# Optimization experiments

Hardware: AMD Instinct MI355X
Metric: run time of the kernel (lower is better)

The kernel has to match this reference:

```python
import jax, jax.numpy as jnp
import numpy as np


def _dense_image_warp(image, flow):
    """Faithful JAX port of tfa.image.dense_image_warp.

    image: [B,H,W,C] float, flow: [B,H,W,2] float (flow[...,0]=dy, flow[...,1]=dx).
    query point (y,x) = grid(y,x) - flow; bilinear interp with TFA's clamping:
    floor clipped to [0, size-2], alpha clipped to [0,1].
    """
    B, H, W, C = image.shape
    gy, gx = jnp.meshgrid(
        jnp.arange(H, dtype=flow.dtype), jnp.arange(W, dtype=flow.dtype), indexing="ij"
    )
    qy = gy[None] - flow[..., 0]  # [B,H,W]
    qx = gx[None] - flow[..., 1]

    y0f = jnp.clip(jnp.floor(qy), 0.0, H - 2)
    x0f = jnp.clip(jnp.floor(qx), 0.0, W - 2)
    ay = jnp.clip(qy - y0f, 0.0, 1.0)[..., None]  # [B,H,W,1]
    ax = jnp.clip(qx - x0f, 0.0, 1.0)[..., None]

    y0 = y0f.astype(jnp.int32)
    x0 = x0f.astype(jnp.int32)
    b = jnp.arange(B, dtype=jnp.int32)[:, None, None]

    tl = image[b, y0, x0]          # top-left  [B,H,W,C]
    tr = image[b, y0, x0 + 1]      # top-right
    bl = image[b, y0 + 1, x0]      # bottom-left
    br = image[b, y0 + 1, x0 + 1]  # bottom-right

    top = tl + ax * (tr - tl)
    bot = bl + ax * (br - bl)
    return top + ay * (bot - top)


def setup_inputs() -> dict:
    key = jax.random.key(0)
    k1, k2 = jax.random.split(key)
    B, H, W, C = 8, 1024, 768, 3
    image = jax.random.normal(k1, (B, H, W, C), dtype=jnp.float32)
    # flow magnitudes of a few pixels, typical for appearance-flow warping
    flow = jax.random.normal(k2, (B, H, W, 2), dtype=jnp.float32) * 5.0
    return {"image": image, "flow": flow}


def reference(image, flow):
    return _dense_image_warp(image, flow)
```

## Files before the change

kernel.cpp:

```cpp
#include <hip/hip_runtime.h>


constexpr int B = 8;
constexpr int H = 1024;
constexpr int W = 768;
constexpr int C = 3;

constexpr int TY = 32, TX = 32;
constexpr int WIN_ROWS = 65;
constexpr int WIN_COLS = 64;
constexpr int WSTRIDE = WIN_COLS * C;
constexpr int CHUNKS  = WIN_ROWS * (WSTRIDE / 4);
constexpr int TILES_X = W / TX;
constexpr int TILES_Y = H / TY;
constexpr int TILES_PER_B = TILES_X * TILES_Y;

constexpr int NTHREADS = 512;
constexpr int PX_PER_T = (TY * TX) / NTHREADS;

typedef float vfloat2 __attribute__((ext_vector_type(2)));
typedef float vfloat4 __attribute__((ext_vector_type(4)));
typedef float vfloat2_a4 __attribute__((ext_vector_type(2), aligned(4)));
typedef float vfloat4_a4 __attribute__((ext_vector_type(4), aligned(4)));

__global__ __launch_bounds__(NTHREADS, 6) void warp_kernel(
    const float* __restrict__ image,
    const float* __restrict__ flow,
    float* __restrict__ out)
{
    __shared__ float win[WIN_ROWS * WSTRIDE + 64];

    const int flat = blockIdx.x;
    const int b    = flat & 7;
    const int s    = flat >> 3;
    const int ty   = s / TILES_X;
    const int tx   = s - ty * TILES_X;
    const int Y0 = ty * TY, X0 = tx * TX;

    const int rowLo = min(max(Y0 - 16, 0), H - WIN_ROWS);
    const int colLo = min(max((X0 - 15) & ~3, 0), W - WIN_COLS);

    const int lane = threadIdx.x & 63;
    const int wv   = threadIdx.x >> 6;

    const float* gwin = image + ((size_t)b * H + rowLo) * (W * C) + colLo * C;
#pragma unroll 1
    for (int j = wv; j * 64 < CHUNKS; j += 8) {
        int ci = j * 64 + lane;
        if (ci >= CHUNKS) ci = CHUNKS - 1;
        const int r = ci / 48;
        const int c = ci - r * 48;
        const float* g = gwin + (size_t)r * (W * C) + c * 4;
        __builtin_amdgcn_global_load_lds(
            (const __attribute__((address_space(1))) void*)g,
            (__attribute__((address_space(3))) void*)(win + (size_t)j * 256),
            16, 0, 0);
    }

    vfloat2 f[PX_PER_T];
#pragma unroll
    for (int k = 0; k < PX_PER_T; ++k) {
        const int p   = threadIdx.x + k * NTHREADS;
        const int py  = p >> 5;
        const int pxx = p & 31;
        const size_t pix = ((size_t)b * H + (Y0 + py)) * W + (X0 + pxx);
        f[k] = __builtin_nontemporal_load((const vfloat2*)flow + pix);
    }

    __syncthreads();

#pragma unroll
    for (int k = 0; k < PX_PER_T; ++k) {
        const int p   = threadIdx.x + k * NTHREADS;
        const int py  = p >> 5;
        const int pxx = p & 31;
        const int y = Y0 + py;
        const int x = X0 + pxx;
        const size_t pix = ((size_t)b * H + y) * W + x;

        const float qy = (float)y - f[k].x;
        const float qx = (float)x - f[k].y;

        float y0f = floorf(qy);
        float x0f = floorf(qx);
        y0f = fminf(fmaxf(y0f, 0.0f), (float)(H - 2));
        x0f = fminf(fmaxf(x0f, 0.0f), (float)(W - 2));
        const float ay = fminf(fmaxf(qy - y0f, 0.0f), 1.0f);
        const float ax = fminf(fmaxf(qx - x0f, 0.0f), 1.0f);

        const int y0 = (int)y0f;
        const int x0 = (int)x0f;

        float tl0, tl1, tl2, tr0, tr1, tr2, bl0, bl1, bl2, br0, br1, br2;

        const bool inwin = (y0 >= rowLo) & (y0 <= rowLo + WIN_ROWS - 2) &
                           (x0 >= colLo) & (x0 <= colLo + WIN_COLS - 2);
        if (inwin) {
            const float* t = &win[(y0 - rowLo) * WSTRIDE + (x0 - colLo) * C];
            tl0 = t[0]; tl1 = t[1]; tl2 = t[2];
            tr0 = t[3]; tr1 = t[4]; tr2 = t[5];
            const float* bo = t + WSTRIDE;
            bl0 = bo[0]; bl1 = bo[1]; bl2 = bo[2];
            br0 = bo[3]; br1 = bo[4]; br2 = bo[5];
        } else {
            const float* top = image + (((size_t)b * H + y0) * W + x0) * C;
            const float* bot = top + (size_t)W * C;
            const vfloat4 t4 = *(const vfloat4_a4*)top;
            const vfloat2 t2 = *(const vfloat2_a4*)(top + 4);
            const vfloat4 b4 = *(const vfloat4_a4*)bot;
            const vfloat2 b2 = *(const vfloat2_a4*)(bot + 4);
            tl0 = t4.x; tl1 = t4.y; tl2 = t4.z;
            tr0 = t4.w; tr1 = t2.x; tr2 = t2.y;
            bl0 = b4.x; bl1 = b4.y; bl2 = b4.z;
            br0 = b4.w; br1 = b2.x; br2 = b2.y;
        }

        const float tp0 = tl0 + ax * (tr0 - tl0);
        const float tp1 = tl1 + ax * (tr1 - tl1);
        const float tp2 = tl2 + ax * (tr2 - tl2);
        const float bo0 = bl0 + ax * (br0 - bl0);
        const float bo1 = bl1 + ax * (br1 - bl1);
        const float bo2 = bl2 + ax * (br2 - bl2);

        float* o = out + pix * C;
        __builtin_nontemporal_store(tp0 + ay * (bo0 - tp0), &o[0]);
        __builtin_nontemporal_store(tp1 + ay * (bo1 - tp1), &o[1]);
        __builtin_nontemporal_store(tp2 + ay * (bo2 - tp2), &o[2]);
    }
}

extern "C" void kernel_launch(void* const* d_in, const int* in_sizes, int n_in,
                              void* d_out, int out_size, void* d_ws, size_t ws_size,
                              hipStream_t stream) {
    const float* image = (const float*)d_in[0];
    const float* flow  = (const float*)d_in[1];
    float* out = (float*)d_out;

    dim3 grid(B * TILES_PER_B);
    dim3 block(NTHREADS);
    warp_kernel<<<grid, block, 0, stream>>>(image, flow, out);
}
```

Measured before the change: 176.1 us.

## Stream column strips through an LDS ring buffer with prefetched row bands

```diff
diff --git a/kernel.cpp b/kernel.cpp
--- a/kernel.cpp
+++ b/kernel.cpp
@@ -6,80 +6,91 @@
 constexpr int W = 768;
 constexpr int C = 3;
 
-constexpr int TY = 32, TX = 32;
-constexpr int WIN_ROWS = 65;
+constexpr int TY = 32;
+constexpr int TX = 24;
+constexpr int TILES_Y = H / TY;
+constexpr int COLS_X  = W / TX;
+
 constexpr int WIN_COLS = 64;
-constexpr int WSTRIDE = WIN_COLS * C;
-constexpr int CHUNKS  = WIN_ROWS * (WSTRIDE / 4);
-constexpr int TILES_X = W / TX;
-constexpr int TILES_Y = H / TY;
-constexpr int TILES_PER_B = TILES_X * TILES_Y;
+constexpr int WSF = WIN_COLS * C;
+constexpr int ROW_CHUNKS = WSF / 4;
+constexpr int BAND = TY;
+constexpr int RING_ROWS = 4 * BAND;
+constexpr int BAND_GROUPS = BAND * ROW_CHUNKS / 64;
+constexpr int NTHREADS = TY * TX;
+constexpr int NWAVES = NTHREADS / 64;
+constexpr int GPW = BAND_GROUPS / NWAVES;
 
-constexpr int NTHREADS = 512;
-constexpr int PX_PER_T = (TY * TX) / NTHREADS;
+static_assert(GPW * NWAVES == BAND_GROUPS, "uniform staging required for vmcnt");
 
 typedef float vfloat2 __attribute__((ext_vector_type(2)));
 typedef float vfloat4 __attribute__((ext_vector_type(4)));
 typedef float vfloat2_a4 __attribute__((ext_vector_type(2), aligned(4)));
 typedef float vfloat4_a4 __attribute__((ext_vector_type(4), aligned(4)));
 
-__global__ __launch_bounds__(NTHREADS, 6) void warp_kernel(
+__global__ __launch_bounds__(NTHREADS) void warp_kernel(
     const float* __restrict__ image,
     const float* __restrict__ flow,
     float* __restrict__ out)
 {
-    __shared__ float win[WIN_ROWS * WSTRIDE + 64];
+    __shared__ float win[RING_ROWS * WSF];
 
-    const int flat = blockIdx.x;
-    const int b    = flat & 7;
-    const int s    = flat >> 3;
-    const int ty   = s / TILES_X;
-    const int tx   = s - ty * TILES_X;
-    const int Y0 = ty * TY, X0 = tx * TX;
-
-    const int rowLo = min(max(Y0 - 16, 0), H - WIN_ROWS);
-    const int colLo = min(max((X0 - 15) & ~3, 0), W - WIN_COLS);
+    const int b  = blockIdx.x & 7;
+    const int tx = blockIdx.x >> 3;
+    const int X0 = tx * TX;
+    const int colLo = min(max(X0 - 20, 0), W - WIN_COLS);
 
     const int lane = threadIdx.x & 63;
     const int wv   = threadIdx.x >> 6;
 
-    const float* gwin = image + ((size_t)b * H + rowLo) * (W * C) + colLo * C;
+    const int py  = threadIdx.x / TX;
+    const int pxx = threadIdx.x - py * TX;
+    const int xg  = X0 + pxx;
+    const float xgf = (float)xg;
+
+    const float* gcol = image + (size_t)b * H * (W * C) + colLo * C;
+
+    auto stage_band = [&](int k) {
+        const int slotBase = (k & 3) * BAND;
+#pragma unroll
+        for (int i = 0; i < GPW; ++i) {
+            const int j  = i * NWAVES + wv;
+            const int ci = j * 64 + lane;
+            const int r  = ci / ROW_CHUNKS;
+            const int c  = ci - r * ROW_CHUNKS;
+            const int rimg = min(k * BAND + r, H - 1);
+            const float* g = gcol + (size_t)rimg * (W * C) + c * 4;
+            __builtin_amdgcn_global_load_lds(
+                (const __attribute__((address_space(1))) void*)g,
+                (__attribute__((address_space(3))) void*)(win + slotBase * WSF + j * 256),
+                16, 0, 0);
+        }
+    };
+
+    auto load_flow = [&](int t) -> vfloat2 {
+        const int yf = min(t * TY + py, H - 1);
+        return __builtin_nontemporal_load(
+            (const vfloat2*)flow + (((size_t)b * H + yf) * W + xg));
+    };
+
+    stage_band(0);
+    stage_band(1);
+    vfloat2 fcur = load_flow(0);
+
 #pragma unroll 1
-    for (int j = wv; j * 64 < CHUNKS; j += 8) {
-        int ci = j * 64 + lane;
-        if (ci >= CHUNKS) ci = CHUNKS - 1;
-        const int r = ci / 48;
-        const int c = ci - r * 48;
-        const float* g = gwin + (size_t)r * (W * C) + c * 4;
-        __builtin_amdgcn_global_load_lds(
-            (const __attribute__((address_space(1))) void*)g,
-            (__attribute__((address_space(3))) void*)(win + (size_t)j * 256),
-            16, 0, 0);
-    }
+    for (int t = 0; t < TILES_Y; ++t) {
+        stage_band(t + 2);
+        const vfloat2 fnxt = load_flow(t + 1);
 
-    vfloat2 f[PX_PER_T];
-#pragma unroll
-    for (int k = 0; k < PX_PER_T; ++k) {
-        const int p   = threadIdx.x + k * NTHREADS;
-        const int py  = p >> 5;
-        const int pxx = p & 31;
-        const size_t pix = ((size_t)b * H + (Y0 + py)) * W + (X0 + pxx);
-        f[k] = __builtin_nontemporal_load((const vfloat2*)flow + pix);
-    }
+        asm volatile("s_waitcnt vmcnt(3)" ::: "memory");
+        __builtin_amdgcn_s_barrier();
+        __builtin_amdgcn_sched_barrier(0);
 
-    __syncthreads();
+        const int Y0 = t * TY;
+        const int y  = Y0 + py;
 
-#pragma unroll
-    for (int k = 0; k < PX_PER_T; ++k) {
-        const int p   = threadIdx.x + k * NTHREADS;
-        const int py  = p >> 5;
-        const int pxx = p & 31;
-        const int y = Y0 + py;
-        const int x = X0 + pxx;
-        const size_t pix = ((size_t)b * H + y) * W + x;
-
-        const float qy = (float)y - f[k].x;
-        const float qx = (float)x - f[k].y;
+        const float qy = (float)y - fcur.x;
+        const float qx = xgf      - fcur.y;
 
         float y0f = floorf(qy);
         float x0f = floorf(qx);
@@ -87,21 +98,20 @@
         x0f = fminf(fmaxf(x0f, 0.0f), (float)(W - 2));
         const float ay = fminf(fmaxf(qy - y0f, 0.0f), 1.0f);
         const float ax = fminf(fmaxf(qx - x0f, 0.0f), 1.0f);
-
         const int y0 = (int)y0f;
         const int x0 = (int)x0f;
 
         float tl0, tl1, tl2, tr0, tr1, tr2, bl0, bl1, bl2, br0, br1, br2;
 
-        const bool inwin = (y0 >= rowLo) & (y0 <= rowLo + WIN_ROWS - 2) &
+        const bool inwin = (y0 >= Y0 - BAND) & (y0 <= Y0 + 2 * BAND - 2) &
                            (x0 >= colLo) & (x0 <= colLo + WIN_COLS - 2);
         if (inwin) {
-            const float* t = &win[(y0 - rowLo) * WSTRIDE + (x0 - colLo) * C];
-            tl0 = t[0]; tl1 = t[1]; tl2 = t[2];
-            tr0 = t[3]; tr1 = t[4]; tr2 = t[5];
-            const float* bo = t + WSTRIDE;
-            bl0 = bo[0]; bl1 = bo[1]; bl2 = bo[2];
-            br0 = bo[3]; br1 = bo[4]; br2 = bo[5];
+            const float* tp = &win[(y0 & (RING_ROWS - 1)) * WSF + (x0 - colLo) * C];
+            const float* bp = &win[((y0 + 1) & (RING_ROWS - 1)) * WSF + (x0 - colLo) * C];
+            tl0 = tp[0]; tl1 = tp[1]; tl2 = tp[2];
+            tr0 = tp[3]; tr1 = tp[4]; tr2 = tp[5];
+            bl0 = bp[0]; bl1 = bp[1]; bl2 = bp[2];
+            br0 = bp[3]; br1 = bp[4]; br2 = bp[5];
         } else {
             const float* top = image + (((size_t)b * H + y0) * W + x0) * C;
             const float* bot = top + (size_t)W * C;
@@ -122,10 +132,14 @@
         const float bo1 = bl1 + ax * (br1 - bl1);
         const float bo2 = bl2 + ax * (br2 - bl2);
 
-        float* o = out + pix * C;
+        float* o = out + (((size_t)b * H + y) * W + xg) * C;
         __builtin_nontemporal_store(tp0 + ay * (bo0 - tp0), &o[0]);
         __builtin_nontemporal_store(tp1 + ay * (bo1 - tp1), &o[1]);
         __builtin_nontemporal_store(tp2 + ay * (bo2 - tp2), &o[2]);
+
+        __builtin_amdgcn_s_barrier();
+        __builtin_amdgcn_sched_barrier(0);
+        fcur = fnxt;
     }
 }
 
@@ -136,7 +150,7 @@
     const float* flow  = (const float*)d_in[1];
     float* out = (float*)d_out;
 
-    dim3 grid(B * TILES_PER_B);
+    dim3 grid(B * COLS_X);
     dim3 block(NTHREADS);
     warp_kernel<<<grid, block, 0, stream>>>(image, flow, out);
 }
```

New measurement: 192.1 us. 1.09x slower.

## Drop LDS window staging and gather bilinear corners directly from global memory

Applied to the files above, without the earlier changes.

```diff
diff --git a/kernel.cpp b/kernel.cpp
--- a/kernel.cpp
+++ b/kernel.cpp
@@ -7,10 +7,6 @@
 constexpr int C = 3;
 
 constexpr int TY = 32, TX = 32;
-constexpr int WIN_ROWS = 65;
-constexpr int WIN_COLS = 64;
-constexpr int WSTRIDE = WIN_COLS * C;
-constexpr int CHUNKS  = WIN_ROWS * (WSTRIDE / 4);
 constexpr int TILES_X = W / TX;
 constexpr int TILES_Y = H / TY;
 constexpr int TILES_PER_B = TILES_X * TILES_Y;
@@ -23,13 +19,11 @@
 typedef float vfloat2_a4 __attribute__((ext_vector_type(2), aligned(4)));
 typedef float vfloat4_a4 __attribute__((ext_vector_type(4), aligned(4)));
 
-__global__ __launch_bounds__(NTHREADS, 6) void warp_kernel(
+__global__ __launch_bounds__(NTHREADS, 8) void warp_kernel(
     const float* __restrict__ image,
     const float* __restrict__ flow,
     float* __restrict__ out)
 {
-    __shared__ float win[WIN_ROWS * WSTRIDE + 64];
-
     const int flat = blockIdx.x;
     const int b    = flat & 7;
     const int s    = flat >> 3;
@@ -37,95 +31,59 @@
     const int tx   = s - ty * TILES_X;
     const int Y0 = ty * TY, X0 = tx * TX;
 
-    const int rowLo = min(max(Y0 - 16, 0), H - WIN_ROWS);
-    const int colLo = min(max((X0 - 15) & ~3, 0), W - WIN_COLS);
+    const float* imgB = image + (size_t)b * H * (W * C);
 
-    const int lane = threadIdx.x & 63;
-    const int wv   = threadIdx.x >> 6;
-
-    const float* gwin = image + ((size_t)b * H + rowLo) * (W * C) + colLo * C;
-#pragma unroll 1
-    for (int j = wv; j * 64 < CHUNKS; j += 8) {
-        int ci = j * 64 + lane;
-        if (ci >= CHUNKS) ci = CHUNKS - 1;
-        const int r = ci / 48;
-        const int c = ci - r * 48;
-        const float* g = gwin + (size_t)r * (W * C) + c * 4;
-        __builtin_amdgcn_global_load_lds(
-            (const __attribute__((address_space(1))) void*)g,
-            (__attribute__((address_space(3))) void*)(win + (size_t)j * 256),
-            16, 0, 0);
-    }
-
+    int yy[PX_PER_T], xx[PX_PER_T];
     vfloat2 f[PX_PER_T];
 #pragma unroll
     for (int k = 0; k < PX_PER_T; ++k) {
-        const int p   = threadIdx.x + k * NTHREADS;
-        const int py  = p >> 5;
-        const int pxx = p & 31;
-        const size_t pix = ((size_t)b * H + (Y0 + py)) * W + (X0 + pxx);
-        f[k] = __builtin_nontemporal_load((const vfloat2*)flow + pix);
+        const int p = threadIdx.x + k * NTHREADS;
+        yy[k] = Y0 + (p >> 5);
+        xx[k] = X0 + (p & 31);
+        f[k] = __builtin_nontemporal_load(
+            (const vfloat2*)flow + (((size_t)b * H + yy[k]) * W + xx[k]));
     }
 
-    __syncthreads();
-
+    vfloat4 t4[PX_PER_T], b4[PX_PER_T];
+    vfloat2 t2[PX_PER_T], b2[PX_PER_T];
+    float ax[PX_PER_T], ay[PX_PER_T];
 #pragma unroll
     for (int k = 0; k < PX_PER_T; ++k) {
-        const int p   = threadIdx.x + k * NTHREADS;
-        const int py  = p >> 5;
-        const int pxx = p & 31;
-        const int y = Y0 + py;
-        const int x = X0 + pxx;
-        const size_t pix = ((size_t)b * H + y) * W + x;
-
-        const float qy = (float)y - f[k].x;
-        const float qx = (float)x - f[k].y;
-
+        const float qy = (float)yy[k] - f[k].x;
+        const float qx = (float)xx[k] - f[k].y;
         float y0f = floorf(qy);
         float x0f = floorf(qx);
         y0f = fminf(fmaxf(y0f, 0.0f), (float)(H - 2));
         x0f = fminf(fmaxf(x0f, 0.0f), (float)(W - 2));
-        const float ay = fminf(fmaxf(qy - y0f, 0.0f), 1.0f);
-        const float ax = fminf(fmaxf(qx - x0f, 0.0f), 1.0f);
+        ay[k] = fminf(fmaxf(qy - y0f, 0.0f), 1.0f);
+        ax[k] = fminf(fmaxf(qx - x0f, 0.0f), 1.0f);
 
-        const int y0 = (int)y0f;
-        const int x0 = (int)x0f;
+        const float* top = imgB + ((size_t)(int)y0f * W + (int)x0f) * C;
+        const float* bot = top + (size_t)W * C;
+        t4[k] = *(const vfloat4_a4*)top;
+        t2[k] = *(const vfloat2_a4*)(top + 4);
+        b4[k] = *(const vfloat4_a4*)bot;
+        b2[k] = *(const vfloat2_a4*)(bot + 4);
+    }
 
-        float tl0, tl1, tl2, tr0, tr1, tr2, bl0, bl1, bl2, br0, br1, br2;
+#pragma unroll
+    for (int k = 0; k < PX_PER_T; ++k) {
+        const float tl0 = t4[k].x, tl1 = t4[k].y, tl2 = t4[k].z;
+        const float tr0 = t4[k].w, tr1 = t2[k].x, tr2 = t2[k].y;
+        const float bl0 = b4[k].x, bl1 = b4[k].y, bl2 = b4[k].z;
+        const float br0 = b4[k].w, br1 = b2[k].x, br2 = b2[k].y;
 
-        const bool inwin = (y0 >= rowLo) & (y0 <= rowLo + WIN_ROWS - 2) &
-                           (x0 >= colLo) & (x0 <= colLo + WIN_COLS - 2);
-        if (inwin) {
-            const float* t = &win[(y0 - rowLo) * WSTRIDE + (x0 - colLo) * C];
-            tl0 = t[0]; tl1 = t[1]; tl2 = t[2];
-            tr0 = t[3]; tr1 = t[4]; tr2 = t[5];
-            const float* bo = t + WSTRIDE;
-            bl0 = bo[0]; bl1 = bo[1]; bl2 = bo[2];
-            br0 = bo[3]; br1 = bo[4]; br2 = bo[5];
-        } else {
-            const float* top = image + (((size_t)b * H + y0) * W + x0) * C;
-            const float* bot = top + (size_t)W * C;
-            const vfloat4 t4 = *(const vfloat4_a4*)top;
-            const vfloat2 t2 = *(const vfloat2_a4*)(top + 4);
-            const vfloat4 b4 = *(const vfloat4_a4*)bot;
-            const vfloat2 b2 = *(const vfloat2_a4*)(bot + 4);
-            tl0 = t4.x; tl1 = t4.y; tl2 = t4.z;
-            tr0 = t4.w; tr1 = t2.x; tr2 = t2.y;
-            bl0 = b4.x; bl1 = b4.y; bl2 = b4.z;
-            br0 = b4.w; br1 = b2.x; br2 = b2.y;
-        }
+        const float tp0 = tl0 + ax[k] * (tr0 - tl0);
+        const float tp1 = tl1 + ax[k] * (tr1 - tl1);
+        const float tp2 = tl2 + ax[k] * (tr2 - tl2);
+        const float bo0 = bl0 + ax[k] * (br0 - bl0);
+        const float bo1 = bl1 + ax[k] * (br1 - bl1);
+        const float bo2 = bl2 + ax[k] * (br2 - bl2);
 
-        const float tp0 = tl0 + ax * (tr0 - tl0);
-        const float tp1 = tl1 + ax * (tr1 - tl1);
-        const float tp2 = tl2 + ax * (tr2 - tl2);
-        const float bo0 = bl0 + ax * (br0 - bl0);
-        const float bo1 = bl1 + ax * (br1 - bl1);
-        const float bo2 = bl2 + ax * (br2 - bl2);
-
-        float* o = out + pix * C;
-        __builtin_nontemporal_store(tp0 + ay * (bo0 - tp0), &o[0]);
-        __builtin_nontemporal_store(tp1 + ay * (bo1 - tp1), &o[1]);
-        __builtin_nontemporal_store(tp2 + ay * (bo2 - tp2), &o[2]);
+        float* o = out + (((size_t)b * H + yy[k]) * W + xx[k]) * C;
+        __builtin_nontemporal_store(tp0 + ay[k] * (bo0 - tp0), &o[0]);
+        __builtin_nontemporal_store(tp1 + ay[k] * (bo1 - tp1), &o[1]);
+        __builtin_nontemporal_store(tp2 + ay[k] * (bo2 - tp2), &o[2]);
     }
 }
 
```

Result: slower. 197.9 us (+12.4%).

## Stage window as padded float4 pixels in LDS via register loads

Applied to the files above, without the earlier changes.

```diff
diff --git a/kernel.cpp b/kernel.cpp
--- a/kernel.cpp
+++ b/kernel.cpp
@@ -9,13 +9,14 @@
 constexpr int TY = 32, TX = 32;
 constexpr int WIN_ROWS = 65;
 constexpr int WIN_COLS = 64;
-constexpr int WSTRIDE = WIN_COLS * C;
-constexpr int CHUNKS  = WIN_ROWS * (WSTRIDE / 4);
+constexpr int LSTRIDE = WIN_COLS + 1;
+constexpr int WIN_PX = WIN_ROWS * WIN_COLS;
 constexpr int TILES_X = W / TX;
 constexpr int TILES_Y = H / TY;
 constexpr int TILES_PER_B = TILES_X * TILES_Y;
 
 constexpr int NTHREADS = 512;
+constexpr int SITER = (WIN_PX + NTHREADS - 1) / NTHREADS;
 constexpr int PX_PER_T = (TY * TX) / NTHREADS;
 
 typedef float vfloat2 __attribute__((ext_vector_type(2)));
@@ -23,12 +24,12 @@
 typedef float vfloat2_a4 __attribute__((ext_vector_type(2), aligned(4)));
 typedef float vfloat4_a4 __attribute__((ext_vector_type(4), aligned(4)));
 
-__global__ __launch_bounds__(NTHREADS, 6) void warp_kernel(
+__global__ __launch_bounds__(NTHREADS, 4) void warp_kernel(
     const float* __restrict__ image,
     const float* __restrict__ flow,
     float* __restrict__ out)
 {
-    __shared__ float win[WIN_ROWS * WSTRIDE + 64];
+    __shared__ vfloat4 win4[WIN_ROWS * LSTRIDE];
 
     const int flat = blockIdx.x;
     const int b    = flat & 7;
@@ -38,23 +39,19 @@
     const int Y0 = ty * TY, X0 = tx * TX;
 
     const int rowLo = min(max(Y0 - 16, 0), H - WIN_ROWS);
-    const int colLo = min(max((X0 - 15) & ~3, 0), W - WIN_COLS);
-
-    const int lane = threadIdx.x & 63;
-    const int wv   = threadIdx.x >> 6;
+    const int colLo = min(max(X0 - 16, 0), W - WIN_COLS);
 
     const float* gwin = image + ((size_t)b * H + rowLo) * (W * C) + colLo * C;
-#pragma unroll 1
-    for (int j = wv; j * 64 < CHUNKS; j += 8) {
-        int ci = j * 64 + lane;
-        if (ci >= CHUNKS) ci = CHUNKS - 1;
-        const int r = ci / 48;
-        const int c = ci - r * 48;
-        const float* g = gwin + (size_t)r * (W * C) + c * 4;
-        __builtin_amdgcn_global_load_lds(
-            (const __attribute__((address_space(1))) void*)g,
-            (__attribute__((address_space(3))) void*)(win + (size_t)j * 256),
-            16, 0, 0);
+    float sr[SITER], sg[SITER], sb[SITER];
+#pragma unroll
+    for (int i = 0; i < SITER; ++i) {
+        const int p = threadIdx.x + i * NTHREADS;
+        if (i < SITER - 1 || p < WIN_PX) {
+            const int r = p >> 6;
+            const int c = p & 63;
+            const float* g = gwin + r * (W * C) + c * 3;
+            sr[i] = g[0]; sg[i] = g[1]; sb[i] = g[2];
+        }
     }
 
     vfloat2 f[PX_PER_T];
@@ -65,6 +62,16 @@
         const int pxx = p & 31;
         const size_t pix = ((size_t)b * H + (Y0 + py)) * W + (X0 + pxx);
         f[k] = __builtin_nontemporal_load((const vfloat2*)flow + pix);
+    }
+
+#pragma unroll
+    for (int i = 0; i < SITER; ++i) {
+        const int p = threadIdx.x + i * NTHREADS;
+        if (i < SITER - 1 || p < WIN_PX) {
+            const int r = p >> 6;
+            const int c = p & 63;
+            win4[r * LSTRIDE + c] = (vfloat4){sr[i], sg[i], sb[i], 0.0f};
+        }
     }
 
     __syncthreads();
@@ -96,12 +103,15 @@
         const bool inwin = (y0 >= rowLo) & (y0 <= rowLo + WIN_ROWS - 2) &
                            (x0 >= colLo) & (x0 <= colLo + WIN_COLS - 2);
         if (inwin) {
-            const float* t = &win[(y0 - rowLo) * WSTRIDE + (x0 - colLo) * C];
-            tl0 = t[0]; tl1 = t[1]; tl2 = t[2];
-            tr0 = t[3]; tr1 = t[4]; tr2 = t[5];
-            const float* bo = t + WSTRIDE;
-            bl0 = bo[0]; bl1 = bo[1]; bl2 = bo[2];
-            br0 = bo[3]; br1 = bo[4]; br2 = bo[5];
+            const int idx = (y0 - rowLo) * LSTRIDE + (x0 - colLo);
+            const vfloat4 tl = win4[idx];
+            const vfloat4 tr = win4[idx + 1];
+            const vfloat4 bl = win4[idx + LSTRIDE];
+            const vfloat4 br = win4[idx + LSTRIDE + 1];
+            tl0 = tl.x; tl1 = tl.y; tl2 = tl.z;
+            tr0 = tr.x; tr1 = tr.y; tr2 = tr.z;
+            bl0 = bl.x; bl1 = bl.y; bl2 = bl.z;
+            br0 = br.x; br1 = br.y; br2 = br.z;
         } else {
             const float* top = image + (((size_t)b * H + y0) * W + x0) * C;
             const float* bot = top + (size_t)W * C;
```

New measurement: 183.4 us. 4.2% more time.
